# Performance work log

Measured on AMD Instinct MI355X. Metric: run time of the kernel, lower is better.

Reference implementation:

```python
import jax, jax.numpy as jnp
import numpy as np

PAD_IDX = 1  # matches init_kwargs pad_idx
TLEN, BATCH, D_IN = 50, 16, 512
SRC_LEN, VOCAB, CVOCAB = 200, 20000, 20400


def setup_inputs() -> dict:
    key = jax.random.key(0)
    k1, k2, k3, k4, k5, k6, k7 = jax.random.split(key, 7)
    hidden = jax.random.normal(k1, (TLEN, BATCH, D_IN), dtype=jnp.float32)
    attn = jax.random.uniform(k2, (TLEN, BATCH, SRC_LEN), dtype=jnp.float32)
    # src_map is a sparse one-hot indicator: each source position maps to one extended-vocab id
    src_ids = jax.random.randint(k3, (SRC_LEN, BATCH), 0, CVOCAB)
    src_map = jax.nn.one_hot(src_ids, CVOCAB, dtype=jnp.float32)  # (src_len, batch, cvocab)
    s = 1.0 / np.sqrt(D_IN)
    W = jax.random.uniform(k4, (VOCAB, D_IN), dtype=jnp.float32, minval=-s, maxval=s)
    b = jax.random.uniform(k5, (VOCAB,), dtype=jnp.float32, minval=-s, maxval=s)
    Wc = jax.random.uniform(k6, (1, D_IN), dtype=jnp.float32, minval=-s, maxval=s)
    bc = jax.random.uniform(k7, (1,), dtype=jnp.float32, minval=-s, maxval=s)
    return {"hidden": hidden, "attn": attn, "src_map": src_map, "W": W, "b": b, "Wc": Wc, "bc": bc}


def reference(hidden, attn, src_map, W, b, Wc, bc):
    tlen, batch, _ = hidden.shape
    src_len, _, cvocab = src_map.shape
    logits = jnp.einsum('tbd,vd->tbv', hidden, W) + b            # (tlen, batch, vocab)
    # faithful to torch: logits[:, pad_idx] = -inf (indexes the batch dim!)
    logits = logits.at[:, PAD_IDX, :].set(-jnp.inf)
    prob = jax.nn.softmax(logits, axis=1)                        # softmax over dim 1, as in source
    p_copy = jax.nn.sigmoid(jnp.einsum('tbd,od->tbo', hidden, Wc) + bc)  # (tlen, batch, 1)
    out_prob = prob * (1.0 - p_copy)                             # (tlen, batch, vocab)
    mul_attn = attn * p_copy                                     # (tlen, batch, src_len)
    # bmm over batch with one-hot src_map: effectively a scatter-add into extended vocab
    copy_prob = jnp.einsum('tbs,sbv->tbv', mul_attn, src_map)    # (tlen, batch, cvocab)
    # faithful to the split/stack/transpose permutation in the source
    flat = copy_prob.reshape(tlen * batch, cvocab)
    copy_prob = flat.reshape(batch, tlen, cvocab).swapaxes(0, 1) # (tlen, batch, cvocab)
    copy_prob = copy_prob.at[:, :, :out_prob.shape[2]].add(out_prob)
    return copy_prob
```

## Files before the change

kernel.cpp:

```cpp
#include <hip/hip_runtime.h>
#include <cstdint>
#include <cstddef>

#define TLEN    50
#define BATCH   16
#define D_IN    512
#define SRC_LEN 200
#define VOCAB   20000
#define CVOCAB  20400

typedef __bf16 bf16x8 __attribute__((ext_vector_type(8)));
typedef float  f32x4  __attribute__((ext_vector_type(4)));

#define GEMM_BLOCKS 625
#define ZERO_BLOCKS 40
#define SCAN_BLOCKS (SRC_LEN * BATCH)
#define NT 256

__global__ __launch_bounds__(256)
void pc_kernel(const float* __restrict__ hidden,
               const float* __restrict__ Wc,
               const float* __restrict__ bc,
               float* __restrict__ pc,
               __bf16* __restrict__ hbf)
{
    const int row  = blockIdx.x * 4 + (threadIdx.x >> 6);
    const int lane = threadIdx.x & 63;
    const float* h = hidden + (size_t)row * D_IN + lane * 8;
    float4 h0 = *(const float4*)(h);
    float4 h1 = *(const float4*)(h + 4);
    bf16x8 hb;
    hb[0] = (__bf16)h0.x; hb[1] = (__bf16)h0.y;
    hb[2] = (__bf16)h0.z; hb[3] = (__bf16)h0.w;
    hb[4] = (__bf16)h1.x; hb[5] = (__bf16)h1.y;
    hb[6] = (__bf16)h1.z; hb[7] = (__bf16)h1.w;
    *(bf16x8*)(hbf + (size_t)row * D_IN + lane * 8) = hb;

    float4 w0 = *(const float4*)(Wc + lane * 8);
    float4 w1 = *(const float4*)(Wc + lane * 8 + 4);
    float s = h0.x*w0.x + h0.y*w0.y + h0.z*w0.z + h0.w*w0.w
            + h1.x*w1.x + h1.y*w1.y + h1.z*w1.z + h1.w*w1.w;
    #pragma unroll
    for (int o = 1; o < 64; o <<= 1) s += __shfl_xor(s, o);
    if (lane == 0) pc[row] = 1.0f / (1.0f + __expf(-(s + bc[0])));
}

__global__ __launch_bounds__(NT)
void fused_main(const __bf16* __restrict__ hbf,
                const float* __restrict__ src_map,
                const float* __restrict__ W,
                const float* __restrict__ pc,
                float* __restrict__ out,
                int* __restrict__ src_ids)
{
    const int bid = blockIdx.x;
    const int tid = threadIdx.x;

    if (bid < GEMM_BLOCKS) {
        __shared__ __align__(16) __bf16 Blds[2 * 16 * 64 * 8];

        const int lane = tid & 63;
        const int wv   = tid >> 6;
        const int l15  = lane & 15;
        const int q    = lane >> 4;
        const int colbase = bid * 32;

        {
            #pragma unroll
            for (int j = 0; j < 8; ++j) {
                const int p = wv * 8 + j;
                const int g = p >> 4;
                const int c = p & 15;
                const float* src = W + (size_t)(colbase + g * 16 + l15) * D_IN
                                     + q * 8 + c * 32;
                float4 f0 = *(const float4*)(src);
                float4 f1 = *(const float4*)(src + 4);
                bf16x8 bf;
                bf[0] = (__bf16)f0.x; bf[1] = (__bf16)f0.y;
                bf[2] = (__bf16)f0.z; bf[3] = (__bf16)f0.w;
                bf[4] = (__bf16)f1.x; bf[5] = (__bf16)f1.y;
                bf[6] = (__bf16)f1.z; bf[7] = (__bf16)f1.w;
                *(bf16x8*)(Blds + (size_t)(g * 16 + c) * 512 + lane * 8) = bf;
            }
        }
        __syncthreads();

        const int tb0 = wv * 12 + (wv < 2 ? wv : 2);
        const int tb1 = tb0 + (wv < 2 ? 13 : 12);

        for (int t = tb0; t < tb1; ++t) {
            const __bf16* arow = hbf + ((size_t)t * BATCH + l15) * D_IN + q * 8;
            f32x4 acc0 = {0.f, 0.f, 0.f, 0.f};
            f32x4 acc1 = {0.f, 0.f, 0.f, 0.f};
            #pragma unroll
            for (int c = 0; c < 16; ++c) {
                bf16x8 af = *(const bf16x8*)(arow + c * 32);
                bf16x8 b0 = *(const bf16x8*)(Blds + (size_t)c * 512 + lane * 8);
                bf16x8 b1 = *(const bf16x8*)(Blds + (size_t)(16 + c) * 512 + lane * 8);
                acc0 = __builtin_amdgcn_mfma_f32_16x16x32_bf16(af, b0, acc0, 0, 0, 0);
                acc1 = __builtin_amdgcn_mfma_f32_16x16x32_bf16(af, b1, acc1, 0, 0, 0);
            }

            float4 pc4 = *(const float4*)(pc + t * 16 + q * 4);

            #pragma unroll
            for (int g = 0; g < 2; ++g) {
                f32x4 acc = g ? acc1 : acc0;
                float mx = -INFINITY;
                #pragma unroll
                for (int r = 0; r < 4; ++r)
                    if (q * 4 + r != 1) mx = fmaxf(mx, acc[r]);
                mx = fmaxf(mx, __shfl_xor(mx, 16));
                mx = fmaxf(mx, __shfl_xor(mx, 32));
                float e[4], s = 0.f;
                #pragma unroll
                for (int r = 0; r < 4; ++r) {
                    e[r] = (q * 4 + r == 1) ? 0.f : __expf(acc[r] - mx);
                    s += e[r];
                }
                s += __shfl_xor(s, 16);
                s += __shfl_xor(s, 32);
                const float inv = 1.0f / s;
                const int v = colbase + g * 16 + l15;
                #pragma unroll
                for (int r = 0; r < 4; ++r) {
                    const int b = q * 4 + r;
                    out[(size_t)(t * BATCH + b) * CVOCAB + v] =
                        e[r] * inv * (1.0f - pc4[r]);
                }
            }
        }
    } else if (bid < GEMM_BLOCKS + ZERO_BLOCKS) {
        const int zb = bid - GEMM_BLOCKS;
        const float4 z = {0.f, 0.f, 0.f, 0.f};
        for (int i = tid; i < 2000; i += NT) {
            const int f = zb * 2000 + i;
            const int r = f / 100;
            const int c = f % 100;
            *(float4*)(out + (size_t)r * CVOCAB + VOCAB + c * 4) = z;
        }
    } else {
        const int row = bid - GEMM_BLOCKS - ZERO_BLOCKS;
        const float4* base = (const float4*)(src_map + (size_t)row * CVOCAB);
        int found = -1;
        for (int i0 = tid; i0 < 1275; i0 += NT) {
            float4 x0 = base[i0];
            float4 x1 = base[i0 + 1275];
            float4 x2 = base[i0 + 2550];
            float4 x3 = base[i0 + 3825];
            #pragma unroll
            for (int seg = 0; seg < 4; ++seg) {
                float4 x = seg == 0 ? x0 : seg == 1 ? x1 : seg == 2 ? x2 : x3;
                const int e0 = (i0 + seg * 1275) * 4;
                if (x.x > 0.5f) found = e0;
                if (x.y > 0.5f) found = e0 + 1;
                if (x.z > 0.5f) found = e0 + 2;
                if (x.w > 0.5f) found = e0 + 3;
            }
        }
        if (found >= 0) src_ids[row] = found;
    }
}

__global__ __launch_bounds__(256)
void scatter_copy(const float* __restrict__ attn,
                  const float* __restrict__ pc,
                  const int* __restrict__ src_ids,
                  float* __restrict__ out)
{
    const int p  = blockIdx.x;
    const int si = threadIdx.x;
    if (si >= SRC_LEN) return;
    const int b  = p & 15;
    const size_t obase = (size_t)((p % TLEN) * BATCH + (p / TLEN)) * CVOCAB;
    const int id = src_ids[si * BATCH + b];
    const float val = attn[(size_t)p * SRC_LEN + si] * pc[p];
    if ((unsigned)id < (unsigned)CVOCAB)
        atomicAdd(out + obase + id, val);
}

extern "C" void kernel_launch(void* const* d_in, const int* in_sizes, int n_in,
                              void* d_out, int out_size, void* d_ws, size_t ws_size,
                              hipStream_t stream)
{
    const float* hidden  = (const float*)d_in[0];
    const float* attn    = (const float*)d_in[1];
    const float* src_map = (const float*)d_in[2];
    const float* W       = (const float*)d_in[3];
    const float* Wc      = (const float*)d_in[5];
    const float* bc      = (const float*)d_in[6];
    float* out   = (float*)d_out;

    int*    src_ids = (int*)d_ws;
    float*  pc      = (float*)((char*)d_ws + 12800);
    __bf16* hbf     = (__bf16*)((char*)d_ws + 16000);

    pc_kernel<<<dim3(200), dim3(256), 0, stream>>>(hidden, Wc, bc, pc, hbf);
    fused_main<<<dim3(GEMM_BLOCKS + ZERO_BLOCKS + SCAN_BLOCKS), dim3(NT), 0, stream>>>(
        hbf, src_map, W, pc, out, src_ids);
    scatter_copy<<<dim3(TLEN * BATCH), dim3(256), 0, stream>>>(attn, pc, src_ids, out);
}
```

Measured before the change: 464.2 us.

## Split fused kernel into scan and GEMM kernels, unroll time pairs in GEMM

Splits the heterogeneous fused kernel into a separate scan/zero kernel and a dedicated GEMM kernel. The GEMM now processes two time steps per iteration, so each shared-memory B fragment feeds four MFMAs instead of two. The scan loads all 20 float4s per thread up front to raise memory-level parallelism. This adds a kernel launch and serialises scan before GEMM, giving up the overlap the fused grid had, and the unrolled loop uses more registers.

```diff
diff --git a/kernel.cpp b/kernel.cpp
--- a/kernel.cpp
+++ b/kernel.cpp
@@ -13,9 +13,8 @@
 typedef float  f32x4  __attribute__((ext_vector_type(4)));
 
 #define GEMM_BLOCKS 625
+#define SCAN_BLOCKS (SRC_LEN * BATCH)
 #define ZERO_BLOCKS 40
-#define SCAN_BLOCKS (SRC_LEN * BATCH)
-#define NT 256
 
 __global__ __launch_bounds__(256)
 void pc_kernel(const float* __restrict__ hidden,
@@ -45,120 +44,139 @@
     if (lane == 0) pc[row] = 1.0f / (1.0f + __expf(-(s + bc[0])));
 }
 
-__global__ __launch_bounds__(NT)
-void fused_main(const __bf16* __restrict__ hbf,
-                const float* __restrict__ src_map,
-                const float* __restrict__ W,
-                const float* __restrict__ pc,
-                float* __restrict__ out,
-                int* __restrict__ src_ids)
+__global__ __launch_bounds__(256)
+void scan_kernel(const float* __restrict__ src_map,
+                 int* __restrict__ src_ids,
+                 float* __restrict__ out)
 {
     const int bid = blockIdx.x;
     const int tid = threadIdx.x;
-
-    if (bid < GEMM_BLOCKS) {
-        __shared__ __align__(16) __bf16 Blds[2 * 16 * 64 * 8];
-
-        const int lane = tid & 63;
-        const int wv   = tid >> 6;
-        const int l15  = lane & 15;
-        const int q    = lane >> 4;
-        const int colbase = bid * 32;
-
-        {
-            #pragma unroll
-            for (int j = 0; j < 8; ++j) {
-                const int p = wv * 8 + j;
-                const int g = p >> 4;
-                const int c = p & 15;
-                const float* src = W + (size_t)(colbase + g * 16 + l15) * D_IN
-                                     + q * 8 + c * 32;
-                float4 f0 = *(const float4*)(src);
-                float4 f1 = *(const float4*)(src + 4);
-                bf16x8 bf;
-                bf[0] = (__bf16)f0.x; bf[1] = (__bf16)f0.y;
-                bf[2] = (__bf16)f0.z; bf[3] = (__bf16)f0.w;
-                bf[4] = (__bf16)f1.x; bf[5] = (__bf16)f1.y;
-                bf[6] = (__bf16)f1.z; bf[7] = (__bf16)f1.w;
-                *(bf16x8*)(Blds + (size_t)(g * 16 + c) * 512 + lane * 8) = bf;
-            }
-        }
-        __syncthreads();
-
-        const int tb0 = wv * 12 + (wv < 2 ? wv : 2);
-        const int tb1 = tb0 + (wv < 2 ? 13 : 12);
-
-        for (int t = tb0; t < tb1; ++t) {
-            const __bf16* arow = hbf + ((size_t)t * BATCH + l15) * D_IN + q * 8;
-            f32x4 acc0 = {0.f, 0.f, 0.f, 0.f};
-            f32x4 acc1 = {0.f, 0.f, 0.f, 0.f};
-            #pragma unroll
-            for (int c = 0; c < 16; ++c) {
-                bf16x8 af = *(const bf16x8*)(arow + c * 32);
-                bf16x8 b0 = *(const bf16x8*)(Blds + (size_t)c * 512 + lane * 8);
-                bf16x8 b1 = *(const bf16x8*)(Blds + (size_t)(16 + c) * 512 + lane * 8);
-                acc0 = __builtin_amdgcn_mfma_f32_16x16x32_bf16(af, b0, acc0, 0, 0, 0);
-                acc1 = __builtin_amdgcn_mfma_f32_16x16x32_bf16(af, b1, acc1, 0, 0, 0);
-            }
-
-            float4 pc4 = *(const float4*)(pc + t * 16 + q * 4);
-
-            #pragma unroll
-            for (int g = 0; g < 2; ++g) {
-                f32x4 acc = g ? acc1 : acc0;
-                float mx = -INFINITY;
-                #pragma unroll
-                for (int r = 0; r < 4; ++r)
-                    if (q * 4 + r != 1) mx = fmaxf(mx, acc[r]);
-                mx = fmaxf(mx, __shfl_xor(mx, 16));
-                mx = fmaxf(mx, __shfl_xor(mx, 32));
-                float e[4], s = 0.f;
-                #pragma unroll
-                for (int r = 0; r < 4; ++r) {
-                    e[r] = (q * 4 + r == 1) ? 0.f : __expf(acc[r] - mx);
-                    s += e[r];
-                }
-                s += __shfl_xor(s, 16);
-                s += __shfl_xor(s, 32);
-                const float inv = 1.0f / s;
-                const int v = colbase + g * 16 + l15;
-                #pragma unroll
-                for (int r = 0; r < 4; ++r) {
-                    const int b = q * 4 + r;
-                    out[(size_t)(t * BATCH + b) * CVOCAB + v] =
-                        e[r] * inv * (1.0f - pc4[r]);
-                }
-            }
-        }
-    } else if (bid < GEMM_BLOCKS + ZERO_BLOCKS) {
-        const int zb = bid - GEMM_BLOCKS;
+    if (bid < SCAN_BLOCKS) {
+        const float4* base = (const float4*)(src_map + (size_t)bid * CVOCAB);
+        float4 x[20];
+        #pragma unroll
+        for (int k = 0; k < 20; ++k) {
+            const int i = tid + k * 256;
+            x[k] = (i < 5100) ? base[i] : float4{0.f, 0.f, 0.f, 0.f};
+        }
+        int found = -1;
+        #pragma unroll
+        for (int k = 0; k < 20; ++k) {
+            const int e0 = (tid + k * 256) * 4;
+            if (x[k].x > 0.5f) found = e0;
+            if (x[k].y > 0.5f) found = e0 + 1;
+            if (x[k].z > 0.5f) found = e0 + 2;
+            if (x[k].w > 0.5f) found = e0 + 3;
+        }
+        if (found >= 0) src_ids[bid] = found;
+    } else {
+        const int zb = bid - SCAN_BLOCKS;
         const float4 z = {0.f, 0.f, 0.f, 0.f};
-        for (int i = tid; i < 2000; i += NT) {
+        for (int i = tid; i < 2000; i += 256) {
             const int f = zb * 2000 + i;
             const int r = f / 100;
             const int c = f % 100;
             *(float4*)(out + (size_t)r * CVOCAB + VOCAB + c * 4) = z;
         }
-    } else {
-        const int row = bid - GEMM_BLOCKS - ZERO_BLOCKS;
-        const float4* base = (const float4*)(src_map + (size_t)row * CVOCAB);
-        int found = -1;
-        for (int i0 = tid; i0 < 1275; i0 += NT) {
-            float4 x0 = base[i0];
-            float4 x1 = base[i0 + 1275];
-            float4 x2 = base[i0 + 2550];
-            float4 x3 = base[i0 + 3825];
+    }
+}
+
+__global__ __launch_bounds__(256)
+void gemm_kernel(const __bf16* __restrict__ hbf,
+                 const float* __restrict__ W,
+                 const float* __restrict__ pc,
+                 float* __restrict__ out)
+{
+    __shared__ __align__(16) __bf16 Blds[2 * 16 * 64 * 8];
+
+    const int tid  = threadIdx.x;
+    const int lane = tid & 63;
+    const int wv   = tid >> 6;
+    const int l15  = lane & 15;
+    const int q    = lane >> 4;
+    const int colbase = blockIdx.x * 32;
+
+    #pragma unroll
+    for (int j = 0; j < 8; ++j) {
+        const int p = wv * 8 + j;
+        const int g = p >> 4;
+        const int c = p & 15;
+        const float* src = W + (size_t)(colbase + g * 16 + l15) * D_IN + q * 8 + c * 32;
+        float4 f0 = *(const float4*)(src);
+        float4 f1 = *(const float4*)(src + 4);
+        bf16x8 bf;
+        bf[0] = (__bf16)f0.x; bf[1] = (__bf16)f0.y;
+        bf[2] = (__bf16)f0.z; bf[3] = (__bf16)f0.w;
+        bf[4] = (__bf16)f1.x; bf[5] = (__bf16)f1.y;
+        bf[6] = (__bf16)f1.z; bf[7] = (__bf16)f1.w;
+        *(bf16x8*)(Blds + (size_t)(g * 16 + c) * 512 + lane * 8) = bf;
+    }
+    __syncthreads();
+
+    auto epilogue = [&](int t, f32x4 acc0, f32x4 acc1) {
+        float4 pc4 = *(const float4*)(pc + t * 16 + q * 4);
+        #pragma unroll
+        for (int g = 0; g < 2; ++g) {
+            f32x4 acc = g ? acc1 : acc0;
+            float mx = -INFINITY;
             #pragma unroll
-            for (int seg = 0; seg < 4; ++seg) {
-                float4 x = seg == 0 ? x0 : seg == 1 ? x1 : seg == 2 ? x2 : x3;
-                const int e0 = (i0 + seg * 1275) * 4;
-                if (x.x > 0.5f) found = e0;
-                if (x.y > 0.5f) found = e0 + 1;
-                if (x.z > 0.5f) found = e0 + 2;
-                if (x.w > 0.5f) found = e0 + 3;
+            for (int r = 0; r < 4; ++r)
+                if (q * 4 + r != 1) mx = fmaxf(mx, acc[r]);
+            mx = fmaxf(mx, __shfl_xor(mx, 16));
+            mx = fmaxf(mx, __shfl_xor(mx, 32));
+            float e[4], s = 0.f;
+            #pragma unroll
+            for (int r = 0; r < 4; ++r) {
+                e[r] = (q * 4 + r == 1) ? 0.f : __expf(acc[r] - mx);
+                s += e[r];
             }
-        }
-        if (found >= 0) src_ids[row] = found;
+            s += __shfl_xor(s, 16);
+            s += __shfl_xor(s, 32);
+            const float inv = 1.0f / s;
+            const int v = colbase + g * 16 + l15;
+            #pragma unroll
+            for (int r = 0; r < 4; ++r) {
+                const int b = q * 4 + r;
+                out[(size_t)(t * BATCH + b) * CVOCAB + v] = e[r] * inv * (1.0f - pc4[r]);
+            }
+        }
+    };
+
+    const int t0 = wv * 12 + (wv < 2 ? wv : 2);
+    const int t1 = t0 + (wv < 2 ? 13 : 12);
+
+    int t = t0;
+    for (; t + 1 < t1; t += 2) {
+        const __bf16* a0p = hbf + ((size_t)t * BATCH + l15) * D_IN + q * 8;
+        const __bf16* a1p = a0p + (size_t)BATCH * D_IN;
+        f32x4 acc00 = {0.f,0.f,0.f,0.f}, acc01 = {0.f,0.f,0.f,0.f};
+        f32x4 acc10 = {0.f,0.f,0.f,0.f}, acc11 = {0.f,0.f,0.f,0.f};
+        #pragma unroll
+        for (int c = 0; c < 16; ++c) {
+            bf16x8 b0  = *(const bf16x8*)(Blds + (size_t)c * 512 + lane * 8);
+            bf16x8 b1  = *(const bf16x8*)(Blds + (size_t)(16 + c) * 512 + lane * 8);
+            bf16x8 af0 = *(const bf16x8*)(a0p + c * 32);
+            bf16x8 af1 = *(const bf16x8*)(a1p + c * 32);
+            acc00 = __builtin_amdgcn_mfma_f32_16x16x32_bf16(af0, b0, acc00, 0, 0, 0);
+            acc01 = __builtin_amdgcn_mfma_f32_16x16x32_bf16(af0, b1, acc01, 0, 0, 0);
+            acc10 = __builtin_amdgcn_mfma_f32_16x16x32_bf16(af1, b0, acc10, 0, 0, 0);
+            acc11 = __builtin_amdgcn_mfma_f32_16x16x32_bf16(af1, b1, acc11, 0, 0, 0);
+        }
+        epilogue(t, acc00, acc01);
+        epilogue(t + 1, acc10, acc11);
+    }
+    if (t < t1) {
+        const __bf16* a0p = hbf + ((size_t)t * BATCH + l15) * D_IN + q * 8;
+        f32x4 acc0 = {0.f,0.f,0.f,0.f}, acc1 = {0.f,0.f,0.f,0.f};
+        #pragma unroll
+        for (int c = 0; c < 16; ++c) {
+            bf16x8 b0 = *(const bf16x8*)(Blds + (size_t)c * 512 + lane * 8);
+            bf16x8 b1 = *(const bf16x8*)(Blds + (size_t)(16 + c) * 512 + lane * 8);
+            bf16x8 af = *(const bf16x8*)(a0p + c * 32);
+            acc0 = __builtin_amdgcn_mfma_f32_16x16x32_bf16(af, b0, acc0, 0, 0, 0);
+            acc1 = __builtin_amdgcn_mfma_f32_16x16x32_bf16(af, b1, acc1, 0, 0, 0);
+        }
+        epilogue(t, acc0, acc1);
     }
 }
 
@@ -196,7 +214,7 @@
     __bf16* hbf     = (__bf16*)((char*)d_ws + 16000);
 
     pc_kernel<<<dim3(200), dim3(256), 0, stream>>>(hidden, Wc, bc, pc, hbf);
-    fused_main<<<dim3(GEMM_BLOCKS + ZERO_BLOCKS + SCAN_BLOCKS), dim3(NT), 0, stream>>>(
-        hbf, src_map, W, pc, out, src_ids);
+    scan_kernel<<<dim3(SCAN_BLOCKS + ZERO_BLOCKS), dim3(256), 0, stream>>>(src_map, src_ids, out);
+    gemm_kernel<<<dim3(GEMM_BLOCKS), dim3(256), 0, stream>>>(hbf, W, pc, out);
     scatter_copy<<<dim3(TLEN * BATCH), dim3(256), 0, stream>>>(attn, pc, src_ids, out);
 }
```

Result: slower. 506.1 us (+9.0%).
